# Kernel optimization log

Measured on AMD Instinct MI355X. Metric: run time of the kernel, lower is better.

Reference implementation:

```python
import jax, jax.numpy as jnp
import numpy as np

N, E, B = 100000, 1600000, 128
F_E, F_X, F_U, H = 128, 128, 128, 64
F_U_OUT = 128


def setup_inputs() -> dict:
    key = jax.random.key(0)
    ks = jax.random.split(key, 16)
    s = lambda fan_in: 1.0 / np.sqrt(fan_in)
    inp = {
        "x": jax.random.normal(ks[0], (N, F_X), jnp.float32),
        "e": jax.random.normal(ks[1], (E, F_E), jnp.float32),
        "u": jax.random.normal(ks[2], (B, F_U), jnp.float32),
        "edge_index": jax.random.randint(ks[3], (2, E), 0, N, jnp.int64),
        "batch": jnp.sort(jax.random.randint(ks[4], (N,), 0, B, jnp.int64)),
        # attention projection params
        "Wk_e": jax.random.uniform(ks[5], (F_E, H), jnp.float32, -s(F_E), s(F_E)),
        "bk_e": jnp.zeros((H,), jnp.float32),
        "Wq_e": jax.random.uniform(ks[6], (F_U, H), jnp.float32, -s(F_U), s(F_U)),
        "bq_e": jnp.zeros((H,), jnp.float32),
        "Wk_x": jax.random.uniform(ks[7], (F_X, H), jnp.float32, -s(F_X), s(F_X)),
        "bk_x": jnp.zeros((H,), jnp.float32),
        "Wq_x": jax.random.uniform(ks[8], (F_U, H), jnp.float32, -s(F_U), s(F_U)),
        "bq_x": jnp.zeros((H,), jnp.float32),
        # phi_u (model_fn = single Linear)
        "Wu": jax.random.uniform(ks[9], (F_E + F_X + F_U, F_U_OUT), jnp.float32,
                                  -s(F_E + F_X + F_U), s(F_E + F_X + F_U)),
        "bu": jnp.zeros((F_U_OUT,), jnp.float32),
    }
    return inp


def reference(x, e, u, edge_index, batch,
              Wk_e, bk_e, Wq_e, bq_e, Wk_x, bk_x, Wq_x, bq_x, Wu, bu):
    num_graphs = u.shape[0]
    src = edge_index[0]
    e_batch = batch[src]                       # [E] graph id per edge

    # edge attention: sigmoid(<k_e, q_e>) per edge, then scatter-add per graph
    k = e @ Wk_e + bk_e                        # [E, H]
    q = (u @ Wq_e + bq_e)[e_batch]             # [E, H] gather
    a_e = jax.nn.sigmoid(jnp.sum(k * q, axis=-1, keepdims=True))  # [E, 1]
    e_agg = jax.ops.segment_sum(a_e * e, e_batch, num_segments=num_graphs)  # [B, F_E]

    # node attention
    kx = x @ Wk_x + bk_x                       # [N, H]
    qx = (u @ Wq_x + bq_x)[batch]              # [N, H] gather
    a_x = jax.nn.sigmoid(jnp.sum(kx * qx, axis=-1, keepdims=True))  # [N, 1]
    x_agg = jax.ops.segment_sum(a_x * x, batch, num_segments=num_graphs)  # [B, F_X]

    out = jnp.concatenate([x_agg, e_agg, u], axis=1)  # [B, F_X+F_E+F_U]
    return out @ Wu + bu                        # [B, F_U_OUT]
```

## Files before the change

### kernel.cpp

```cpp
#include <hip/hip_runtime.h>
#include <hip/hip_bf16.h>


#define FDIM 128
#define BGRAPH 128
#define HDIM 64
#define SLICES 16
#define CAP 16384
#define CURSOR_STRIDE 16
#define SC_THREADS 512
#define SC_ITEMS 16
#define MAXCHUNK (CAP / SLICES)

typedef float vf4 __attribute__((ext_vector_type(4)));

__device__ inline vf4 ldnt4(const float* p) {
    return __builtin_nontemporal_load(reinterpret_cast<const vf4*>(p));
}

__global__ __launch_bounds__(SC_THREADS) void prep_kernel(
    const int* __restrict__ src, const int* __restrict__ batch,
    int* __restrict__ cursor,
    int* __restrict__ order,
    float* __restrict__ x_agg,
    const float* __restrict__ x,
    const float* __restrict__ u,
    const float* __restrict__ Wk_e, const float* __restrict__ bk_e,
    const float* __restrict__ Wq_e, const float* __restrict__ bq_e,
    const float* __restrict__ Wk_x, const float* __restrict__ bk_x,
    const float* __restrict__ Wq_x, const float* __restrict__ bq_x,
    float* __restrict__ v_e, float* __restrict__ c_e,
    int E, int N, int nb_edge)
{
    const int t = threadIdx.x;

    if (blockIdx.x < nb_edge) {
        __shared__ int lh[BGRAPH];
        __shared__ int s_base[BGRAPH];
        if (t < BGRAPH) lh[t] = 0;
        __syncthreads();

        const int base0 = blockIdx.x * SC_THREADS * SC_ITEMS;
        int gv[SC_ITEMS], rv[SC_ITEMS];
#pragma unroll
        for (int k = 0; k < SC_ITEMS; ++k) {
            const int i = base0 + k * SC_THREADS + t;
            if (i < E) {
                const int g = batch[__builtin_nontemporal_load(src + i)];
                gv[k] = g;
                rv[k] = atomicAdd(&lh[g], 1);
            } else {
                gv[k] = -1; rv[k] = 0;
            }
        }
        __syncthreads();
        if (t < BGRAPH) {
            const int n = lh[t];
            const int b = (n > 0) ? atomicAdd(&cursor[t * CURSOR_STRIDE], n) : 0;
            s_base[t] = t * CAP + b;
        }
        __syncthreads();
#pragma unroll
        for (int k = 0; k < SC_ITEMS; ++k) {
            const int i = base0 + k * SC_THREADS + t;
            if (gv[k] >= 0) order[s_base[gv[k]] + rv[k]] = i;
        }
    } else {
        const int g2  = blockIdx.x - nb_edge;
        const int g   = g2 >> 1;
        const int par = g2 & 1;
        __shared__ float su[FDIM];
        __shared__ float sqe[HDIM];
        __shared__ float sqx[HDIM];
        __shared__ float s_vx[FDIM];
        __shared__ float s_cx;

        if (t < FDIM) su[t] = u[g * FDIM + t];
        __syncthreads();

        if (t < HDIM) {
            float acc = bq_e[t];
            for (int f = 0; f < FDIM; ++f) acc += su[f] * Wq_e[f * HDIM + t];
            sqe[t] = acc;
        } else if (t < 2 * HDIM) {
            const int h = t - HDIM;
            float acc = bq_x[h];
            for (int f = 0; f < FDIM; ++f) acc += su[f] * Wq_x[f * HDIM + h];
            sqx[h] = acc;
        }
        __syncthreads();

        if (t < FDIM) {
            float acce = 0.f, accx = 0.f;
            for (int h = 0; h < HDIM; ++h) {
                acce += Wk_e[t * HDIM + h] * sqe[h];
                accx += Wk_x[t * HDIM + h] * sqx[h];
            }
            if (par == 0) v_e[g * FDIM + t] = acce;
            s_vx[t] = accx;
        }
        if (t == 0) {
            float cx = 0.f;
            for (int h = 0; h < HDIM; ++h) cx += bk_x[h] * sqx[h];
            s_cx = cx;
            if (par == 0) {
                float ce = 0.f;
                for (int h = 0; h < HDIM; ++h) ce += bk_e[h] * sqe[h];
                c_e[g] = ce;
            }
        }
        __syncthreads();

        int lo = 0, hi = N;
        while (lo < hi) { int mid = (lo + hi) >> 1; if (batch[mid] < g) lo = mid + 1; else hi = mid; }
        const int start = lo;
        hi = N;
        while (lo < hi) { int mid = (lo + hi) >> 1; if (batch[mid] < g + 1) lo = mid + 1; else hi = mid; }
        const int end = lo;

        const int hidx = t >> 5;
        const int hl   = t & 31;
        const vf4 fv = *reinterpret_cast<const vf4*>(&s_vx[4 * hl]);
        const float cg = s_cx;

        vf4 acc = (vf4)(0.f);
        int row = start + 2 * hidx + par;
        vf4 fe = (vf4)(0.f);
        if (row < end) fe = ldnt4(x + (size_t)row * FDIM + 4 * hl);
        for (; row < end; row += 32) {
            vf4 fen = (vf4)(0.f);
            if (row + 32 < end) fen = ldnt4(x + (size_t)(row + 32) * FDIM + 4 * hl);
            float d = fe.x * fv.x + fe.y * fv.y + fe.z * fv.z + fe.w * fv.w;
            d += __shfl_xor(d, 1);
            d += __shfl_xor(d, 2);
            d += __shfl_xor(d, 4);
            d += __shfl_xor(d, 8);
            d += __shfl_xor(d, 16);
            const float a = 1.f / (1.f + __expf(-(d + cg)));
            acc.x += a * fe.x; acc.y += a * fe.y; acc.z += a * fe.z; acc.w += a * fe.w;
            fe = fen;
        }

        __shared__ float s_red[16][FDIM];
        s_red[hidx][4 * hl + 0] = acc.x;
        s_red[hidx][4 * hl + 1] = acc.y;
        s_red[hidx][4 * hl + 2] = acc.z;
        s_red[hidx][4 * hl + 3] = acc.w;
        __syncthreads();

        if (t < FDIM) {
            float ssum = 0.f;
#pragma unroll
            for (int k = 0; k < 16; ++k) ssum += s_red[k][t];
            unsafeAtomicAdd(&x_agg[g * FDIM + t], ssum);
        }
    }
}

__global__ __launch_bounds__(1024, 8) void agg_kernel(
    const float* __restrict__ e,
    const int*   __restrict__ order,
    const int*   __restrict__ cursor,
    const float* __restrict__ v_e, const float* __restrict__ c_e,
    float* __restrict__ e_agg)
{
    const int tid  = threadIdx.x;
    const int hidx = tid >> 5;
    const int hl   = tid & 31;
    __shared__ float s_red[32][FDIM];
    __shared__ int s_ids[MAXCHUNK];

    const int g = blockIdx.x / SLICES;
    const int s = blockIdx.x % SLICES;
    const int len = cursor[g * CURSOR_STRIDE];
    const int chunk = (len + SLICES - 1) / SLICES;
    const int clo = s * chunk;
    const int cnt = min(chunk, len - clo);

    for (int i = tid; i < cnt; i += 1024) s_ids[i] = order[g * CAP + clo + i];
    __syncthreads();

    const vf4 fv = *reinterpret_cast<const vf4*>(v_e + g * FDIM + 4 * hl);
    const float cg = c_e[g];

    vf4 acc = (vf4)(0.f);

    int p = hidx;
    vf4 f0 = (vf4)(0.f), f1 = (vf4)(0.f), f2 = (vf4)(0.f);
    if (p < cnt)      f0 = ldnt4(e + (size_t)s_ids[p]      * FDIM + 4 * hl);
    if (p + 32 < cnt) f1 = ldnt4(e + (size_t)s_ids[p + 32] * FDIM + 4 * hl);
    if (p + 64 < cnt) f2 = ldnt4(e + (size_t)s_ids[p + 64] * FDIM + 4 * hl);

    for (; p < cnt; p += 32) {
        vf4 f3 = (vf4)(0.f);
        if (p + 96 < cnt) f3 = ldnt4(e + (size_t)s_ids[p + 96] * FDIM + 4 * hl);

        float d = f0.x * fv.x + f0.y * fv.y + f0.z * fv.z + f0.w * fv.w;
        d += __shfl_xor(d, 1);
        d += __shfl_xor(d, 2);
        d += __shfl_xor(d, 4);
        d += __shfl_xor(d, 8);
        d += __shfl_xor(d, 16);
        const float a = 1.f / (1.f + __expf(-(d + cg)));
        acc.x += a * f0.x; acc.y += a * f0.y; acc.z += a * f0.z; acc.w += a * f0.w;

        f0 = f1; f1 = f2; f2 = f3;
    }

    s_red[hidx][4 * hl + 0] = acc.x;
    s_red[hidx][4 * hl + 1] = acc.y;
    s_red[hidx][4 * hl + 2] = acc.z;
    s_red[hidx][4 * hl + 3] = acc.w;
    __syncthreads();

    if (tid < FDIM) {
        float ssum = 0.f;
#pragma unroll
        for (int k = 0; k < 32; ++k) ssum += s_red[k][tid];
        unsafeAtomicAdd(&e_agg[g * FDIM + tid], ssum);
    }
}

__global__ __launch_bounds__(128) void final_kernel(
    const float* __restrict__ x_agg, const float* __restrict__ e_agg,
    const float* __restrict__ u,
    const float* __restrict__ Wu, const float* __restrict__ bu,
    float* __restrict__ out)
{
    const int g = blockIdx.x;
    const int o = threadIdx.x;
    __shared__ float cat[3 * FDIM];
    cat[o]            = x_agg[g * FDIM + o];
    cat[FDIM + o]     = e_agg[g * FDIM + o];
    cat[2 * FDIM + o] = u[g * FDIM + o];
    __syncthreads();

    float acc = bu[o];
#pragma unroll 8
    for (int r = 0; r < 3 * FDIM; ++r) acc += cat[r] * Wu[r * FDIM + o];
    out[g * FDIM + o] = acc;
}

extern "C" void kernel_launch(void* const* d_in, const int* in_sizes, int n_in,
                              void* d_out, int out_size, void* d_ws, size_t ws_size,
                              hipStream_t stream) {
    const float* x          = (const float*)d_in[0];
    const float* e          = (const float*)d_in[1];
    const float* u          = (const float*)d_in[2];
    const int*   edge_index = (const int*)d_in[3];
    const int*   batch      = (const int*)d_in[4];
    const float* Wk_e = (const float*)d_in[5];
    const float* bk_e = (const float*)d_in[6];
    const float* Wq_e = (const float*)d_in[7];
    const float* bq_e = (const float*)d_in[8];
    const float* Wk_x = (const float*)d_in[9];
    const float* bk_x = (const float*)d_in[10];
    const float* Wq_x = (const float*)d_in[11];
    const float* bq_x = (const float*)d_in[12];
    const float* Wu   = (const float*)d_in[13];
    const float* bu   = (const float*)d_in[14];

    const int N = in_sizes[4];
    const int E = in_sizes[3] / 2;
    const int* src = edge_index;

    float* ws    = (float*)d_ws;
    float* v_e   = ws;
    float* c_e   = v_e + BGRAPH * FDIM;
    float* e_agg = c_e + BGRAPH;
    float* x_agg = e_agg + BGRAPH * FDIM;
    int*   cursor = (int*)(x_agg + BGRAPH * FDIM);
    int*   order  = cursor + BGRAPH * CURSOR_STRIDE;

    hipMemsetAsync(e_agg, 0,
        (2 * BGRAPH * FDIM + BGRAPH * CURSOR_STRIDE) * sizeof(float), stream);

    const int nb_edge = (E + SC_THREADS * SC_ITEMS - 1) / (SC_THREADS * SC_ITEMS);
    prep_kernel<<<nb_edge + 2 * BGRAPH, SC_THREADS, 0, stream>>>(
        src, batch, cursor, order, x_agg, x,
        u, Wk_e, bk_e, Wq_e, bq_e, Wk_x, bk_x, Wq_x, bq_x,
        v_e, c_e, E, N, nb_edge);

    agg_kernel<<<BGRAPH * SLICES, 1024, 0, stream>>>(
        e, order, cursor, v_e, c_e, e_agg);

    final_kernel<<<BGRAPH, 128, 0, stream>>>(
        x_agg, e_agg, u, Wu, bu, (float*)d_out);
}
```

Before: 202.8 us.

## Locally sort edge ids by graph in LDS before coalesced scatter to order

The edge bucketing stage now does a block-local counting sort. A shared-memory prefix scan over per-graph counts is followed by staging edge ids and bin ids in LDS, so that writes to the global order array are contiguous runs per graph rather than scattered per-thread stores. The src and batch loads are also split into separate unrolled loops to raise memory-level parallelism. In exchange it uses about 41KB more shared memory per block and two extra barriers, which may lower occupancy of the prep kernel.

```diff
diff --git a/kernel.cpp b/kernel.cpp
--- a/kernel.cpp
+++ b/kernel.cpp
@@ -10,6 +10,7 @@
 #define CURSOR_STRIDE 16
 #define SC_THREADS 512
 #define SC_ITEMS 16
+#define SC_TOTAL (SC_THREADS * SC_ITEMS)
 #define MAXCHUNK (CAP / SLICES)
 
 typedef float vf4 __attribute__((ext_vector_type(4)));
@@ -36,34 +37,67 @@
 
     if (blockIdx.x < nb_edge) {
         __shared__ int lh[BGRAPH];
-        __shared__ int s_base[BGRAPH];
+        __shared__ int s_lofs[BGRAPH];
+        __shared__ int s_gbase[BGRAPH];
+        __shared__ int wtot[2];
+        __shared__ int s_ids[SC_TOTAL];
+        __shared__ unsigned char s_bin[SC_TOTAL];
+
         if (t < BGRAPH) lh[t] = 0;
         __syncthreads();
 
-        const int base0 = blockIdx.x * SC_THREADS * SC_ITEMS;
-        int gv[SC_ITEMS], rv[SC_ITEMS];
+        const int base0 = blockIdx.x * SC_TOTAL;
+        const int nval_blk = min(SC_TOTAL, E - base0);
+
+        int iv[SC_ITEMS];
 #pragma unroll
         for (int k = 0; k < SC_ITEMS; ++k) {
             const int i = base0 + k * SC_THREADS + t;
-            if (i < E) {
-                const int g = batch[__builtin_nontemporal_load(src + i)];
-                gv[k] = g;
-                rv[k] = atomicAdd(&lh[g], 1);
-            } else {
-                gv[k] = -1; rv[k] = 0;
+            iv[k] = (i < E) ? __builtin_nontemporal_load(src + i) : -1;
+        }
+        int gv[SC_ITEMS];
+#pragma unroll
+        for (int k = 0; k < SC_ITEMS; ++k)
+            gv[k] = (iv[k] >= 0) ? batch[iv[k]] : -1;
+        int rv[SC_ITEMS];
+#pragma unroll
+        for (int k = 0; k < SC_ITEMS; ++k)
+            rv[k] = (gv[k] >= 0) ? atomicAdd(&lh[gv[k]], 1) : 0;
+        __syncthreads();
+
+        if (t < BGRAPH) {
+            const int val = lh[t];
+            int xs = val;
+            for (int off = 1; off < 64; off <<= 1) {
+                const int y = __shfl_up(xs, off, 64);
+                if ((t & 63) >= off) xs += y;
             }
+            if ((t & 63) == 63) wtot[t >> 6] = xs;
+            s_lofs[t] = xs - val;
         }
         __syncthreads();
         if (t < BGRAPH) {
+            const int lofs = s_lofs[t] + ((t >= 64) ? wtot[0] : 0);
+            s_lofs[t] = lofs;
             const int n = lh[t];
-            const int b = (n > 0) ? atomicAdd(&cursor[t * CURSOR_STRIDE], n) : 0;
-            s_base[t] = t * CAP + b;
-        }
-        __syncthreads();
+            const int gb = (n > 0) ? atomicAdd(&cursor[t * CURSOR_STRIDE], n) : 0;
+            s_gbase[t] = t * CAP + gb - lofs;
+        }
+        __syncthreads();
+
 #pragma unroll
         for (int k = 0; k < SC_ITEMS; ++k) {
-            const int i = base0 + k * SC_THREADS + t;
-            if (gv[k] >= 0) order[s_base[gv[k]] + rv[k]] = i;
+            if (gv[k] >= 0) {
+                const int slot = s_lofs[gv[k]] + rv[k];
+                s_ids[slot] = base0 + k * SC_THREADS + t;
+                s_bin[slot] = (unsigned char)gv[k];
+            }
+        }
+        __syncthreads();
+
+        for (int p = t; p < nval_blk; p += SC_THREADS) {
+            const int b = s_bin[p];
+            order[s_gbase[b] + p] = s_ids[p];
         }
     } else {
         const int g2  = blockIdx.x - nb_edge;
@@ -275,7 +309,7 @@
     hipMemsetAsync(e_agg, 0,
         (2 * BGRAPH * FDIM + BGRAPH * CURSOR_STRIDE) * sizeof(float), stream);
 
-    const int nb_edge = (E + SC_THREADS * SC_ITEMS - 1) / (SC_THREADS * SC_ITEMS);
+    const int nb_edge = (E + SC_TOTAL - 1) / SC_TOTAL;
     prep_kernel<<<nb_edge + 2 * BGRAPH, SC_THREADS, 0, stream>>>(
         src, batch, cursor, order, x_agg, x,
         u, Wk_e, bk_e, Wq_e, bq_e, Wk_x, bk_x, Wq_x, bq_x,
```

After: 197.3 us, median of 2. 2.7% less time.
